# Kernel tuning notes

Measured on AMD Instinct MI355X. Metric: run time of the kernel, lower is better.

Reference implementation:

```python
import jax, jax.numpy as jnp
import numpy as np

N = 50000      # nodes
E = 800000     # edges
NFEAT = 128
NHID = 128
EPS = 1e-5     # BatchNorm eps


def setup_inputs() -> dict:
    key = jax.random.key(0)
    ks = jax.random.split(key, 16)
    def lin(k, fan_in, shape):
        return jax.random.uniform(k, shape, jnp.float32, -1.0, 1.0) / np.sqrt(fan_in)
    return {
        "x": jax.random.normal(ks[0], (N, NFEAT), jnp.float32),
        "edge_index": jax.random.randint(ks[1], (2, E), 0, N, jnp.int32),
        "edge_weight": jax.random.uniform(ks[2], (E,), jnp.float32),
        # GCNConv 1 (nfeat -> nhid)
        "W1": lin(ks[3], NFEAT, (NFEAT, NHID)), "b1": jnp.zeros((NHID,), jnp.float32),
        # GCNConv 2 (nhid -> nhid)
        "W2": lin(ks[4], NHID, (NHID, NHID)), "b2": jnp.zeros((NHID,), jnp.float32),
        # BatchNorm affine params
        "g1": jnp.ones((NHID,), jnp.float32), "be1": jnp.zeros((NHID,), jnp.float32),
        "g2": jnp.ones((NHID,), jnp.float32), "be2": jnp.zeros((NHID,), jnp.float32),
        # MLP head: fc1 (nfeat + 2*nhid -> nhid), fc2 (nhid -> 1)
        "Wf1": lin(ks[5], NFEAT + 2 * NHID, (NFEAT + 2 * NHID, NHID)),
        "bf1": lin(ks[6], NFEAT + 2 * NHID, (NHID,)),
        "Wf2": lin(ks[7], NHID, (NHID, 1)),
        "bf2": lin(ks[8], NHID, (1,)),
    }


def _gcn_conv(x, src, dst, w, W, b):
    """PyG GCNConv with add_self_loops=True and symmetric gcn_norm."""
    h = x @ W                                   # [N, out] linear first
    deg = jnp.zeros((N,), h.dtype).at[dst].add(w) + 1.0  # +1 self-loop weight
    dinv = jax.lax.rsqrt(deg)                   # deg^{-1/2}
    norm = dinv[src] * w * dinv[dst]            # [E]
    out = jnp.zeros_like(h).at[dst].add(h[src] * norm[:, None])  # scatter-add
    out = out + h * (dinv * dinv)[:, None]      # self-loop term dinv_i^2 * h_i
    return out + b


def _bn(x, g, b):  # training-mode BatchNorm1d over node dim (biased var)
    m = x.mean(axis=0)
    v = x.var(axis=0)
    return g * (x - m) * jax.lax.rsqrt(v + EPS) + b


def reference(x, edge_index, edge_weight, W1, b1, W2, b2, g1, be1, g2, be2,
              Wf1, bf1, Wf2, bf2):
    src, dst = edge_index[0], edge_index[1]
    h1 = _bn(jax.nn.relu(_gcn_conv(x, src, dst, edge_weight, W1, b1)), g1, be1)
    h2 = _bn(jax.nn.relu(_gcn_conv(h1, src, dst, edge_weight, W2, b2)), g2, be2)
    cat = jnp.concatenate([x, h1, h2], axis=1)          # [N, nfeat+2*nhid]
    out = jax.nn.relu(cat @ Wf1 + bf1)
    out = jax.nn.relu(out @ Wf2 + bf2)
    return out.reshape(-1)                              # [N]
```

## Files before the change

### kernel.cpp

```cpp
#include <hip/hip_runtime.h>
#include <hip/hip_bf16.h>
#include <hip/hip_fp16.h>

#define NN 50000
#define EE 800000
constexpr float BN_EPS = 1e-5f;

typedef float  f32x4  __attribute__((ext_vector_type(4)));
typedef short  s16x8  __attribute__((ext_vector_type(8)));
typedef __bf16 bf16x8 __attribute__((ext_vector_type(8)));

struct __align__(8) Edge { int s; float w; };

__device__ inline void split2(float f, short& h, short& l) {
    unsigned u  = __builtin_bit_cast(unsigned, f);
    unsigned hr = (u + 0x7fffu + ((u >> 16) & 1u)) >> 16;
    h = (short)hr;
    float hf = __builtin_bit_cast(float, hr << 16);
    float r  = f - hf;
    unsigned u2 = __builtin_bit_cast(unsigned, r);
    unsigned lr = (u2 + 0x7fffu + ((u2 >> 16) & 1u)) >> 16;
    l = (short)lr;
}
__device__ inline f32x4 mfma_bf16(s16x8 a, s16x8 b, f32x4 c) {
    return __builtin_amdgcn_mfma_f32_16x16x32_bf16(
        __builtin_bit_cast(bf16x8, a), __builtin_bit_cast(bf16x8, b), c, 0, 0, 0);
}

__global__ __launch_bounds__(256) void k_zero_int(int* p, int n) {
    int i = blockIdx.x * 256 + threadIdx.x;
    if (i < n) p[i] = 0;
}

__global__ __launch_bounds__(256) void k_hist_rank(const int* __restrict__ dst,
                                                   int* __restrict__ cnt,
                                                   int* __restrict__ rank) {
    int e = blockIdx.x * 256 + threadIdx.x;
    if (e < EE) rank[e] = atomicAdd(&cnt[dst[e]], 1);
}
__global__ __launch_bounds__(256) void k_scan1(const int* __restrict__ cnt,
                                               int* __restrict__ excl,
                                               int* __restrict__ blksum) {
    __shared__ int sh[256];
    int tid = threadIdx.x;
    int i = blockIdx.x * 256 + tid;
    int v = (i < NN) ? cnt[i] : 0;
    sh[tid] = v;
    __syncthreads();
    #pragma unroll
    for (int off = 1; off < 256; off <<= 1) {
        int x = (tid >= off) ? sh[tid - off] : 0;
        __syncthreads();
        sh[tid] += x;
        __syncthreads();
    }
    if (i < NN) excl[i] = sh[tid] - v;
    if (tid == 255) blksum[blockIdx.x] = sh[255];
}
__global__ __launch_bounds__(256) void k_scan2(int* blksum, int nblk) {
    __shared__ int sh[256];
    int tid = threadIdx.x;
    sh[tid] = (tid < nblk) ? blksum[tid] : 0;
    __syncthreads();
    #pragma unroll
    for (int off = 1; off < 256; off <<= 1) {
        int x = (tid >= off) ? sh[tid - off] : 0;
        __syncthreads();
        sh[tid] += x;
        __syncthreads();
    }
    if (tid < nblk) blksum[tid] = sh[tid];
}
__global__ __launch_bounds__(256) void k_scan3(const int* __restrict__ excl,
                                               const int* __restrict__ blksum,
                                               int* __restrict__ rowptr) {
    int i = blockIdx.x * 256 + threadIdx.x;
    if (i < NN)
        rowptr[i] = excl[i] + (blockIdx.x > 0 ? blksum[blockIdx.x - 1] : 0);
    if (i == 0) rowptr[NN] = EE;
}
__global__ __launch_bounds__(256) void k_place2(const int* __restrict__ src,
                                                const int* __restrict__ dst,
                                                const float* __restrict__ w,
                                                const int* __restrict__ rowptr,
                                                const int* __restrict__ rank,
                                                Edge* __restrict__ csr_e) {
    int e = blockIdx.x * 256 + threadIdx.x;
    if (e >= EE) return;
    int slot = rowptr[dst[e]] + rank[e];
    Edge ed; ed.s = src[e]; ed.w = w[e];
    csr_e[slot] = ed;
}
__global__ __launch_bounds__(256) void k_deg_dinv(const int* __restrict__ rowptr,
                                                  const Edge* __restrict__ csr_e,
                                                  float* __restrict__ dinv) {
    int i = blockIdx.x * 256 + threadIdx.x;
    if (i >= NN) return;
    int e0 = rowptr[i], e1 = rowptr[i + 1];
    float s = 1.0f;
    for (int e = e0; e < e1; e++) s += csr_e[e].w;
    dinv[i] = rsqrtf(s);
}
__global__ __launch_bounds__(256) void k_edge_coef(Edge* __restrict__ csr_e,
                                                   const float* __restrict__ dinv) {
    int e = blockIdx.x * 256 + threadIdx.x;
    if (e < EE) {
        Edge ed = csr_e[e];
        ed.w *= dinv[ed.s];
        csr_e[e] = ed;
    }
}

__global__ __launch_bounds__(256) void k_cvt_wT(const float* __restrict__ W,
                                                short* __restrict__ Th,
                                                short* __restrict__ Tl, int K) {
    int idx = blockIdx.x * 256 + threadIdx.x;
    if (idx >= K * 128) return;
    int k = idx >> 7, c = idx & 127;
    short h, l;
    split2(W[idx], h, l);
    Th[c * K + k] = h;
    Tl[c * K + k] = l;
}

__global__ __launch_bounds__(256) void gemm_mfma(const float* __restrict__ X,
                                                 const float* __restrict__ sc,
                                                 const float* __restrict__ sh,
                                                 const short* __restrict__ WTh,
                                                 const short* __restrict__ WTl,
                                                 __half* __restrict__ Y, int n) {
    __shared__ __align__(16) short As[2][64][40];
    __shared__ __align__(16) short Bs[2][128][40];
    int tid  = threadIdx.x;
    int row0 = blockIdx.x * 64;
    int w = tid >> 6, lane = tid & 63;
    int wr = w >> 1, wc = w & 1;
    int fr = lane & 15, fq = lane >> 4;
    f32x4 acc[2][4] = {};
    for (int k0 = 0; k0 < 128; k0 += 32) {
        {
            int r = tid >> 2, seg = tid & 3;
            int gr = row0 + r;
            float f[8];
            if (gr < n) {
                float4 v0 = *(const float4*)&X[(size_t)gr * 128 + k0 + seg * 8];
                float4 v1 = *(const float4*)&X[(size_t)gr * 128 + k0 + seg * 8 + 4];
                f[0]=v0.x; f[1]=v0.y; f[2]=v0.z; f[3]=v0.w;
                f[4]=v1.x; f[5]=v1.y; f[6]=v1.z; f[7]=v1.w;
            } else {
                #pragma unroll
                for (int i = 0; i < 8; i++) f[i] = 0.f;
            }
            if (sc) {
                float scv[8], shv[8];
                *(float4*)&scv[0] = *(const float4*)&sc[k0 + seg * 8];
                *(float4*)&scv[4] = *(const float4*)&sc[k0 + seg * 8 + 4];
                *(float4*)&shv[0] = *(const float4*)&sh[k0 + seg * 8];
                *(float4*)&shv[4] = *(const float4*)&sh[k0 + seg * 8 + 4];
                #pragma unroll
                for (int i = 0; i < 8; i++) f[i] = fmaf(f[i], scv[i], shv[i]);
            }
            short h[8], l[8];
            #pragma unroll
            for (int i = 0; i < 8; i++) split2(f[i], h[i], l[i]);
            *(s16x8*)&As[0][r][seg * 8] = *(s16x8*)h;
            *(s16x8*)&As[1][r][seg * 8] = *(s16x8*)l;
        }
        #pragma unroll
        for (int rd = 0; rd < 2; rd++) {
            int idx = rd * 256 + tid;
            int c = idx >> 2, seg = idx & 3;
            *(s16x8*)&Bs[0][c][seg * 8] = *(const s16x8*)&WTh[c * 128 + k0 + seg * 8];
            *(s16x8*)&Bs[1][c][seg * 8] = *(const s16x8*)&WTl[c * 128 + k0 + seg * 8];
        }
        __syncthreads();
        s16x8 ah[2], al[2], bh[4], bl[4];
        #pragma unroll
        for (int m = 0; m < 2; m++) {
            int r = wr * 32 + m * 16 + fr;
            ah[m] = *(s16x8*)&As[0][r][fq * 8];
            al[m] = *(s16x8*)&As[1][r][fq * 8];
        }
        #pragma unroll
        for (int nf = 0; nf < 4; nf++) {
            int c = wc * 64 + nf * 16 + fr;
            bh[nf] = *(s16x8*)&Bs[0][c][fq * 8];
            bl[nf] = *(s16x8*)&Bs[1][c][fq * 8];
        }
        #pragma unroll
        for (int m = 0; m < 2; m++)
            #pragma unroll
            for (int nf = 0; nf < 4; nf++) {
                acc[m][nf] = mfma_bf16(ah[m], bh[nf], acc[m][nf]);
                acc[m][nf] = mfma_bf16(ah[m], bl[nf], acc[m][nf]);
                acc[m][nf] = mfma_bf16(al[m], bh[nf], acc[m][nf]);
            }
        __syncthreads();
    }
    #pragma unroll
    for (int m = 0; m < 2; m++)
        #pragma unroll
        for (int nf = 0; nf < 4; nf++)
            #pragma unroll
            for (int j = 0; j < 4; j++) {
                int gr = row0 + wr * 32 + m * 16 + fq * 4 + j;
                int gc = wc * 64 + nf * 16 + fr;
                if (gr < n) Y[(size_t)gr * 128 + gc] = __float2half(acc[m][nf][j]);
            }
}

__global__ __launch_bounds__(256) void gemm_head_mfma(const float* __restrict__ X0,
                                                      const float* __restrict__ X1,
                                                      const float* __restrict__ X2,
                                                      const float* __restrict__ sc1,
                                                      const float* __restrict__ sh1,
                                                      const float* __restrict__ sc2,
                                                      const float* __restrict__ sh2,
                                                      const short* __restrict__ WTh,
                                                      const short* __restrict__ WTl,
                                                      const float* __restrict__ bf1,
                                                      const float* __restrict__ Wf2,
                                                      const float* __restrict__ bf2,
                                                      float* __restrict__ out) {
    __shared__ __align__(16) short As[2][64][40];
    __shared__ __align__(16) short Bs[2][128][40];
    __shared__ float red[64];
    int tid  = threadIdx.x;
    int row0 = blockIdx.x * 64;
    int w = tid >> 6, lane = tid & 63;
    int wr = w >> 1, wc = w & 1;
    int fr = lane & 15, fq = lane >> 4;
    f32x4 acc[2][4] = {};
    for (int k0 = 0; k0 < 384; k0 += 32) {
        const float* S   = (k0 < 128) ? X0 : (k0 < 256) ? X1 : X2;
        const float* scp = (k0 < 128) ? nullptr : (k0 < 256) ? sc1 : sc2;
        const float* shp = (k0 < 128) ? nullptr : (k0 < 256) ? sh1 : sh2;
        int kb = k0 & 127;
        {
            int r = tid >> 2, seg = tid & 3;
            int gr = row0 + r;
            float f[8];
            if (gr < NN) {
                float4 v0 = *(const float4*)&S[(size_t)gr * 128 + kb + seg * 8];
                float4 v1 = *(const float4*)&S[(size_t)gr * 128 + kb + seg * 8 + 4];
                f[0]=v0.x; f[1]=v0.y; f[2]=v0.z; f[3]=v0.w;
                f[4]=v1.x; f[5]=v1.y; f[6]=v1.z; f[7]=v1.w;
            } else {
                #pragma unroll
                for (int i = 0; i < 8; i++) f[i] = 0.f;
            }
            if (scp) {
                float scv[8], shv[8];
                *(float4*)&scv[0] = *(const float4*)&scp[kb + seg * 8];
                *(float4*)&scv[4] = *(const float4*)&scp[kb + seg * 8 + 4];
                *(float4*)&shv[0] = *(const float4*)&shp[kb + seg * 8];
                *(float4*)&shv[4] = *(const float4*)&shp[kb + seg * 8 + 4];
                #pragma unroll
                for (int i = 0; i < 8; i++) f[i] = fmaf(f[i], scv[i], shv[i]);
            }
            short h[8], l[8];
            #pragma unroll
            for (int i = 0; i < 8; i++) split2(f[i], h[i], l[i]);
            *(s16x8*)&As[0][r][seg * 8] = *(s16x8*)h;
            *(s16x8*)&As[1][r][seg * 8] = *(s16x8*)l;
        }
        #pragma unroll
        for (int rd = 0; rd < 2; rd++) {
            int idx = rd * 256 + tid;
            int c = idx >> 2, seg = idx & 3;
            *(s16x8*)&Bs[0][c][seg * 8] = *(const s16x8*)&WTh[c * 384 + k0 + seg * 8];
            *(s16x8*)&Bs[1][c][seg * 8] = *(const s16x8*)&WTl[c * 384 + k0 + seg * 8];
        }
        __syncthreads();
        s16x8 ah[2], al[2], bh[4], bl[4];
        #pragma unroll
        for (int m = 0; m < 2; m++) {
            int r = wr * 32 + m * 16 + fr;
            ah[m] = *(s16x8*)&As[0][r][fq * 8];
            al[m] = *(s16x8*)&As[1][r][fq * 8];
        }
        #pragma unroll
        for (int nf = 0; nf < 4; nf++) {
            int c = wc * 64 + nf * 16 + fr;
            bh[nf] = *(s16x8*)&Bs[0][c][fq * 8];
            bl[nf] = *(s16x8*)&Bs[1][c][fq * 8];
        }
        #pragma unroll
        for (int m = 0; m < 2; m++)
            #pragma unroll
            for (int nf = 0; nf < 4; nf++) {
                acc[m][nf] = mfma_bf16(ah[m], bh[nf], acc[m][nf]);
                acc[m][nf] = mfma_bf16(ah[m], bl[nf], acc[m][nf]);
                acc[m][nf] = mfma_bf16(al[m], bh[nf], acc[m][nf]);
            }
        __syncthreads();
    }
    if (tid < 64) red[tid] = 0.f;
    __syncthreads();
    float ps[2][4] = {};
    #pragma unroll
    for (int m = 0; m < 2; m++)
        #pragma unroll
        for (int nf = 0; nf < 4; nf++) {
            int gc = wc * 64 + nf * 16 + fr;
            float b1v = bf1[gc];
            float w2v = Wf2[gc];
            #pragma unroll
            for (int j = 0; j < 4; j++) {
                float u = fmaxf(acc[m][nf][j] + b1v, 0.f);
                ps[m][j] = fmaf(u, w2v, ps[m][j]);
            }
        }
    #pragma unroll
    for (int off = 1; off <= 8; off <<= 1)
        #pragma unroll
        for (int m = 0; m < 2; m++)
            #pragma unroll
            for (int j = 0; j < 4; j++)
                ps[m][j] += __shfl_xor(ps[m][j], off, 64);
    if (fr == 0) {
        #pragma unroll
        for (int m = 0; m < 2; m++)
            #pragma unroll
            for (int j = 0; j < 4; j++)
                atomicAdd(&red[wr * 32 + m * 16 + fq * 4 + j], ps[m][j]);
    }
    __syncthreads();
    if (tid < 64 && row0 + tid < NN)
        out[row0 + tid] = fmaxf(red[tid] + bf2[0], 0.f);
}

__global__ __launch_bounds__(256) void k_agg_stats(const __half* __restrict__ t,
                                                   const float* __restrict__ dinv,
                                                   const float* __restrict__ b,
                                                   const int* __restrict__ rowptr,
                                                   const Edge* __restrict__ csr_e,
                                                   float* __restrict__ h,
                                                   float* __restrict__ partS,
                                                   float* __restrict__ partSS) {
    int wv   = threadIdx.x >> 6;
    int lane = threadIdx.x & 63;
    int sub  = lane >> 4;
    int sl   = lane & 15;
    float bb[8];
    *(float4*)&bb[0] = *(const float4*)&b[sl * 8];
    *(float4*)&bb[4] = *(const float4*)&b[sl * 8 + 4];
    float sS[8] = {}, sSS[8] = {};
    #pragma unroll 1
    for (int ni = 0; ni < 8; ni++) {
        int wid = blockIdx.x * 32 + wv * 8 + ni;
        if (wid >= NN) break;
        float di = dinv[wid];
        float acc[8];
        if (sub == 0) {
            s16x8 raw = *(const s16x8*)&t[(size_t)wid * 128 + sl * 8];
            union { s16x8 r; __half2 h2[4]; } u; u.r = raw;
            #pragma unroll
            for (int i = 0; i < 4; i++) {
                float2 f = __half22float2(u.h2[i]);
                acc[2 * i]     = f.x * di;
                acc[2 * i + 1] = f.y * di;
            }
        } else {
            #pragma unroll
            for (int i = 0; i < 8; i++) acc[i] = 0.f;
        }
        int e0 = rowptr[wid], e1 = rowptr[wid + 1];
        #pragma unroll 2
        for (int e = e0; e < e1; e += 4) {
            int ee   = e + sub;
            bool v   = ee < e1;
            int idx  = v ? ee : e0;
            Edge ed  = csr_e[idx];
            float cw = v ? ed.w : 0.f;
            s16x8 raw = *(const s16x8*)&t[(size_t)ed.s * 128 + sl * 8];
            union { s16x8 r; __half2 h2[4]; } u; u.r = raw;
            #pragma unroll
            for (int i = 0; i < 4; i++) {
                float2 f = __half22float2(u.h2[i]);
                acc[2 * i]     = fmaf(f.x, cw, acc[2 * i]);
                acc[2 * i + 1] = fmaf(f.y, cw, acc[2 * i + 1]);
            }
        }
        #pragma unroll
        for (int i = 0; i < 8; i++) {
            acc[i] += __shfl_xor(acc[i], 16, 64);
            acc[i] += __shfl_xor(acc[i], 32, 64);
        }
        if (sub == 0) {
            float hv[8];
            #pragma unroll
            for (int i = 0; i < 8; i++) {
                hv[i] = fmaxf(fmaf(acc[i], di, bb[i]), 0.f);
                sS[i]  += hv[i];
                sSS[i] += hv[i] * hv[i];
            }
            *(float4*)&h[(size_t)wid * 128 + sl * 8]     = *(float4*)&hv[0];
            *(float4*)&h[(size_t)wid * 128 + sl * 8 + 4] = *(float4*)&hv[4];
        }
    }
    __shared__ float s_s[4][128], s_ss[4][128];
    if (sub == 0) {
        #pragma unroll
        for (int i = 0; i < 8; i++) {
            s_s [wv][sl * 8 + i] = sS[i];
            s_ss[wv][sl * 8 + i] = sSS[i];
        }
    }
    __syncthreads();
    if (threadIdx.x < 128) {
        int c = threadIdx.x;
        float S  = s_s [0][c] + s_s [1][c] + s_s [2][c] + s_s [3][c];
        float SS = s_ss[0][c] + s_ss[1][c] + s_ss[2][c] + s_ss[3][c];
        partS [blockIdx.x * 128 + c] = S;
        partSS[blockIdx.x * 128 + c] = SS;
    }
}

__global__ __launch_bounds__(256) void k_stats(const float* __restrict__ partS,
                                               const float* __restrict__ partSS,
                                               int nblk,
                                               const float* __restrict__ g,
                                               const float* __restrict__ be,
                                               float* __restrict__ scale,
                                               float* __restrict__ shift) {
    int c   = blockIdx.x;
    int tid = threadIdx.x;
    float s = 0.f, ss = 0.f;
    for (int b = tid; b < nblk; b += 256) {
        s  += partS [b * 128 + c];
        ss += partSS[b * 128 + c];
    }
    #pragma unroll
    for (int off = 32; off > 0; off >>= 1) {
        s  += __shfl_down(s,  off, 64);
        ss += __shfl_down(ss, off, 64);
    }
    __shared__ float sh_s[4], sh_ss[4];
    int wv = tid >> 6, lane = tid & 63;
    if (lane == 0) { sh_s[wv] = s; sh_ss[wv] = ss; }
    __syncthreads();
    if (tid == 0) {
        float S  = sh_s[0]  + sh_s[1]  + sh_s[2]  + sh_s[3];
        float SS = sh_ss[0] + sh_ss[1] + sh_ss[2] + sh_ss[3];
        float mean = S / (float)NN;
        float var  = SS / (float)NN - mean * mean;
        float sc   = g[c] * rsqrtf(var + BN_EPS);
        scale[c] = sc;
        shift[c] = be[c] - mean * sc;
    }
}

extern "C" void kernel_launch(void* const* d_in, const int* in_sizes, int n_in,
                              void* d_out, int out_size, void* d_ws, size_t ws_size,
                              hipStream_t stream) {
    const float* x   = (const float*)d_in[0];
    const int*   ei  = (const int*)d_in[1];
    const float* ew  = (const float*)d_in[2];
    const float* W1  = (const float*)d_in[3];
    const float* b1  = (const float*)d_in[4];
    const float* W2  = (const float*)d_in[5];
    const float* b2  = (const float*)d_in[6];
    const float* g1  = (const float*)d_in[7];
    const float* be1 = (const float*)d_in[8];
    const float* g2  = (const float*)d_in[9];
    const float* be2 = (const float*)d_in[10];
    const float* Wf1 = (const float*)d_in[11];
    const float* bf1 = (const float*)d_in[12];
    const float* Wf2 = (const float*)d_in[13];
    const float* bf2 = (const float*)d_in[14];
    float* out = (float*)d_out;

    const int* src = ei;
    const int* dst = ei + EE;

    const int NAGG = (NN + 31) / 32;

    float* w = (float*)d_ws;
    __half* t      = (__half*)w;  w += (size_t)NN * 64;
    float* h1      = w;  w += (size_t)NN * 128;
    float* h2      = w;  w += (size_t)NN * 128;
    float* dinv    = w;  w += 50048;
    float* partS   = w;  w += (size_t)NAGG * 128;
    float* partSS  = w;  w += (size_t)NAGG * 128;
    float* scale1  = w;  w += 128;
    float* shift1  = w;  w += 128;
    float* scale2  = w;  w += 128;
    float* shift2  = w;  w += 128;
    Edge* csr_e    = (Edge*)w;  w += 2 * (size_t)EE;
    int* iw        = (int*)w;
    int* rowptr    = iw; iw += 50056;
    int* cnt       = iw; iw += 50048;
    int* excl      = iw; iw += 50048;
    int* blksum    = iw; iw += 256;
    short* sw      = (short*)iw;
    short* W1th = sw; sw += 128 * 128;
    short* W1tl = sw; sw += 128 * 128;
    short* W2th = sw; sw += 128 * 128;
    short* W2tl = sw; sw += 128 * 128;
    short* Wfth = sw; sw += 128 * 384;
    short* Wftl = sw; sw += 128 * 384;
    int* rank = (int*)t;

    const int GN = (NN + 255) / 256;
    const int GE = (EE + 255) / 256;
    const int NBLK = (NN + 63) / 64;

    k_cvt_wT<<<(128 * 128 + 255) / 256, 256, 0, stream>>>(W1, W1th, W1tl, 128);
    k_cvt_wT<<<(128 * 128 + 255) / 256, 256, 0, stream>>>(W2, W2th, W2tl, 128);
    k_cvt_wT<<<(384 * 128 + 255) / 256, 256, 0, stream>>>(Wf1, Wfth, Wftl, 384);

    k_zero_int<<<GN, 256, 0, stream>>>(cnt, 50048);
    k_hist_rank<<<GE, 256, 0, stream>>>(dst, cnt, rank);
    k_scan1<<<GN, 256, 0, stream>>>(cnt, excl, blksum);
    k_scan2<<<1, 256, 0, stream>>>(blksum, GN);
    k_scan3<<<GN, 256, 0, stream>>>(excl, blksum, rowptr);
    k_place2<<<GE, 256, 0, stream>>>(src, dst, ew, rowptr, rank, csr_e);
    k_deg_dinv<<<GN, 256, 0, stream>>>(rowptr, csr_e, dinv);
    k_edge_coef<<<GE, 256, 0, stream>>>(csr_e, dinv);

    gemm_mfma<<<NBLK, 256, 0, stream>>>(x, nullptr, nullptr, W1th, W1tl, t, NN);
    k_agg_stats<<<NAGG, 256, 0, stream>>>(t, dinv, b1, rowptr, csr_e,
                                          h1, partS, partSS);
    k_stats<<<128, 256, 0, stream>>>(partS, partSS, NAGG, g1, be1, scale1, shift1);

    gemm_mfma<<<NBLK, 256, 0, stream>>>(h1, scale1, shift1, W2th, W2tl, t, NN);
    k_agg_stats<<<NAGG, 256, 0, stream>>>(t, dinv, b2, rowptr, csr_e,
                                          h2, partS, partSS);
    k_stats<<<128, 256, 0, stream>>>(partS, partSS, NAGG, g2, be2, scale2, shift2);

    gemm_head_mfma<<<NBLK, 256, 0, stream>>>(x, h1, h2, scale1, shift1, scale2, shift2,
                                             Wfth, Wftl, bf1, Wf2, bf2, out);
}
```

Before: 227.9 us.

## Store h1/h2 as fp16, merge weight conversions, widen aggregation blocks

Intermediate activations h1 and h2 are now written in fp16 instead of fp32, which halves their write traffic in aggregation and their read traffic in the second GEMM and the head GEMM. The three weight-conversion launches are merged into one kernel. The aggregation kernel now runs 512 threads per block with 8 waves doing 4 nodes each, and its edge loop is unrolled by 4 instead of 2. Rounding the pre-BatchNorm activations to fp16 adds quantization error to the outputs.

```diff
diff --git a/kernel.cpp b/kernel.cpp
--- a/kernel.cpp
+++ b/kernel.cpp
@@ -111,19 +111,63 @@
     }
 }
 
-__global__ __launch_bounds__(256) void k_cvt_wT(const float* __restrict__ W,
-                                                short* __restrict__ Th,
-                                                short* __restrict__ Tl, int K) {
-    int idx = blockIdx.x * 256 + threadIdx.x;
-    if (idx >= K * 128) return;
+__device__ inline void cvt_one(const float* W, short* Th, short* Tl, int idx, int K) {
     int k = idx >> 7, c = idx & 127;
     short h, l;
     split2(W[idx], h, l);
     Th[c * K + k] = h;
     Tl[c * K + k] = l;
 }
-
-__global__ __launch_bounds__(256) void gemm_mfma(const float* __restrict__ X,
+__global__ __launch_bounds__(256) void k_cvt_all(const float* __restrict__ W1,
+                                                 const float* __restrict__ W2,
+                                                 const float* __restrict__ Wf1,
+                                                 short* W1th, short* W1tl,
+                                                 short* W2th, short* W2tl,
+                                                 short* Wfth, short* Wftl) {
+    int idx = blockIdx.x * 256 + threadIdx.x;
+    if (idx < 16384)       cvt_one(W1,  W1th, W1tl, idx, 128);
+    else if (idx < 32768)  cvt_one(W2,  W2th, W2tl, idx - 16384, 128);
+    else if (idx < 81920)  cvt_one(Wf1, Wfth, Wftl, idx - 32768, 384);
+}
+
+__device__ inline void stage_a(const void* X, bool xfp16, const float* sc, const float* sh,
+                               int gr, int n, int kbase, int seg, short* h, short* l) {
+    float f[8];
+    if (gr < n) {
+        if (xfp16) {
+            const __half* Xh = (const __half*)X;
+            s16x8 raw = *(const s16x8*)&Xh[(size_t)gr * 128 + kbase + seg * 8];
+            union { s16x8 r; __half2 h2[4]; } u; u.r = raw;
+            #pragma unroll
+            for (int i = 0; i < 4; i++) {
+                float2 f2 = __half22float2(u.h2[i]);
+                f[2 * i] = f2.x; f[2 * i + 1] = f2.y;
+            }
+        } else {
+            const float* Xf = (const float*)X;
+            float4 v0 = *(const float4*)&Xf[(size_t)gr * 128 + kbase + seg * 8];
+            float4 v1 = *(const float4*)&Xf[(size_t)gr * 128 + kbase + seg * 8 + 4];
+            f[0]=v0.x; f[1]=v0.y; f[2]=v0.z; f[3]=v0.w;
+            f[4]=v1.x; f[5]=v1.y; f[6]=v1.z; f[7]=v1.w;
+        }
+    } else {
+        #pragma unroll
+        for (int i = 0; i < 8; i++) f[i] = 0.f;
+    }
+    if (sc) {
+        float scv[8], shv[8];
+        *(float4*)&scv[0] = *(const float4*)&sc[kbase + seg * 8];
+        *(float4*)&scv[4] = *(const float4*)&sc[kbase + seg * 8 + 4];
+        *(float4*)&shv[0] = *(const float4*)&sh[kbase + seg * 8];
+        *(float4*)&shv[4] = *(const float4*)&sh[kbase + seg * 8 + 4];
+        #pragma unroll
+        for (int i = 0; i < 8; i++) f[i] = fmaf(f[i], scv[i], shv[i]);
+    }
+    #pragma unroll
+    for (int i = 0; i < 8; i++) split2(f[i], h[i], l[i]);
+}
+
+__global__ __launch_bounds__(256) void gemm_mfma(const void* __restrict__ X, int xfp16,
                                                  const float* __restrict__ sc,
                                                  const float* __restrict__ sh,
                                                  const short* __restrict__ WTh,
@@ -140,29 +184,8 @@
     for (int k0 = 0; k0 < 128; k0 += 32) {
         {
             int r = tid >> 2, seg = tid & 3;
-            int gr = row0 + r;
-            float f[8];
-            if (gr < n) {
-                float4 v0 = *(const float4*)&X[(size_t)gr * 128 + k0 + seg * 8];
-                float4 v1 = *(const float4*)&X[(size_t)gr * 128 + k0 + seg * 8 + 4];
-                f[0]=v0.x; f[1]=v0.y; f[2]=v0.z; f[3]=v0.w;
-                f[4]=v1.x; f[5]=v1.y; f[6]=v1.z; f[7]=v1.w;
-            } else {
-                #pragma unroll
-                for (int i = 0; i < 8; i++) f[i] = 0.f;
-            }
-            if (sc) {
-                float scv[8], shv[8];
-                *(float4*)&scv[0] = *(const float4*)&sc[k0 + seg * 8];
-                *(float4*)&scv[4] = *(const float4*)&sc[k0 + seg * 8 + 4];
-                *(float4*)&shv[0] = *(const float4*)&sh[k0 + seg * 8];
-                *(float4*)&shv[4] = *(const float4*)&sh[k0 + seg * 8 + 4];
-                #pragma unroll
-                for (int i = 0; i < 8; i++) f[i] = fmaf(f[i], scv[i], shv[i]);
-            }
             short h[8], l[8];
-            #pragma unroll
-            for (int i = 0; i < 8; i++) split2(f[i], h[i], l[i]);
+            stage_a(X, xfp16 != 0, sc, sh, row0 + r, n, k0, seg, h, l);
             *(s16x8*)&As[0][r][seg * 8] = *(s16x8*)h;
             *(s16x8*)&As[1][r][seg * 8] = *(s16x8*)l;
         }
@@ -210,8 +233,8 @@
 }
 
 __global__ __launch_bounds__(256) void gemm_head_mfma(const float* __restrict__ X0,
-                                                      const float* __restrict__ X1,
-                                                      const float* __restrict__ X2,
+                                                      const __half* __restrict__ X1,
+                                                      const __half* __restrict__ X2,
                                                       const float* __restrict__ sc1,
                                                       const float* __restrict__ sh1,
                                                       const float* __restrict__ sc2,
@@ -232,35 +255,15 @@
     int fr = lane & 15, fq = lane >> 4;
     f32x4 acc[2][4] = {};
     for (int k0 = 0; k0 < 384; k0 += 32) {
-        const float* S   = (k0 < 128) ? X0 : (k0 < 256) ? X1 : X2;
-        const float* scp = (k0 < 128) ? nullptr : (k0 < 256) ? sc1 : sc2;
-        const float* shp = (k0 < 128) ? nullptr : (k0 < 256) ? sh1 : sh2;
+        const void*  S     = (k0 < 128) ? (const void*)X0 : (k0 < 256) ? (const void*)X1 : (const void*)X2;
+        bool         sfp16 = (k0 >= 128);
+        const float* scp   = (k0 < 128) ? nullptr : (k0 < 256) ? sc1 : sc2;
+        const float* shp   = (k0 < 128) ? nullptr : (k0 < 256) ? sh1 : sh2;
         int kb = k0 & 127;
         {
             int r = tid >> 2, seg = tid & 3;
-            int gr = row0 + r;
-            float f[8];
-            if (gr < NN) {
-                float4 v0 = *(const float4*)&S[(size_t)gr * 128 + kb + seg * 8];
-                float4 v1 = *(const float4*)&S[(size_t)gr * 128 + kb + seg * 8 + 4];
-                f[0]=v0.x; f[1]=v0.y; f[2]=v0.z; f[3]=v0.w;
-                f[4]=v1.x; f[5]=v1.y; f[6]=v1.z; f[7]=v1.w;
-            } else {
-                #pragma unroll
-                for (int i = 0; i < 8; i++) f[i] = 0.f;
-            }
-            if (scp) {
-                float scv[8], shv[8];
-                *(float4*)&scv[0] = *(const float4*)&scp[kb + seg * 8];
-                *(float4*)&scv[4] = *(const float4*)&scp[kb + seg * 8 + 4];
-                *(float4*)&shv[0] = *(const float4*)&shp[kb + seg * 8];
-                *(float4*)&shv[4] = *(const float4*)&shp[kb + seg * 8 + 4];
-                #pragma unroll
-                for (int i = 0; i < 8; i++) f[i] = fmaf(f[i], scv[i], shv[i]);
-            }
             short h[8], l[8];
-            #pragma unroll
-            for (int i = 0; i < 8; i++) split2(f[i], h[i], l[i]);
+            stage_a(S, sfp16, scp, shp, row0 + r, NN, kb, seg, h, l);
             *(s16x8*)&As[0][r][seg * 8] = *(s16x8*)h;
             *(s16x8*)&As[1][r][seg * 8] = *(s16x8*)l;
         }
@@ -330,12 +333,12 @@
         out[row0 + tid] = fmaxf(red[tid] + bf2[0], 0.f);
 }
 
-__global__ __launch_bounds__(256) void k_agg_stats(const __half* __restrict__ t,
+__global__ __launch_bounds__(512) void k_agg_stats(const __half* __restrict__ t,
                                                    const float* __restrict__ dinv,
                                                    const float* __restrict__ b,
                                                    const int* __restrict__ rowptr,
                                                    const Edge* __restrict__ csr_e,
-                                                   float* __restrict__ h,
+                                                   __half* __restrict__ h,
                                                    float* __restrict__ partS,
                                                    float* __restrict__ partSS) {
     int wv   = threadIdx.x >> 6;
@@ -347,8 +350,8 @@
     *(float4*)&bb[4] = *(const float4*)&b[sl * 8 + 4];
     float sS[8] = {}, sSS[8] = {};
     #pragma unroll 1
-    for (int ni = 0; ni < 8; ni++) {
-        int wid = blockIdx.x * 32 + wv * 8 + ni;
+    for (int ni = 0; ni < 4; ni++) {
+        int wid = blockIdx.x * 32 + wv * 4 + ni;
         if (wid >= NN) break;
         float di = dinv[wid];
         float acc[8];
@@ -366,12 +369,11 @@
             for (int i = 0; i < 8; i++) acc[i] = 0.f;
         }
         int e0 = rowptr[wid], e1 = rowptr[wid + 1];
-        #pragma unroll 2
+        #pragma unroll 4
         for (int e = e0; e < e1; e += 4) {
             int ee   = e + sub;
             bool v   = ee < e1;
-            int idx  = v ? ee : e0;
-            Edge ed  = csr_e[idx];
+            Edge ed  = csr_e[v ? ee : e0];
             float cw = v ? ed.w : 0.f;
             s16x8 raw = *(const s16x8*)&t[(size_t)ed.s * 128 + sl * 8];
             union { s16x8 r; __half2 h2[4]; } u; u.r = raw;
@@ -389,17 +391,20 @@
         }
         if (sub == 0) {
             float hv[8];
+            union { s16x8 r; __half2 h2[4]; } o;
             #pragma unroll
             for (int i = 0; i < 8; i++) {
                 hv[i] = fmaxf(fmaf(acc[i], di, bb[i]), 0.f);
                 sS[i]  += hv[i];
                 sSS[i] += hv[i] * hv[i];
             }
-            *(float4*)&h[(size_t)wid * 128 + sl * 8]     = *(float4*)&hv[0];
-            *(float4*)&h[(size_t)wid * 128 + sl * 8 + 4] = *(float4*)&hv[4];
-        }
-    }
-    __shared__ float s_s[4][128], s_ss[4][128];
+            #pragma unroll
+            for (int i = 0; i < 4; i++)
+                o.h2[i] = __floats2half2_rn(hv[2 * i], hv[2 * i + 1]);
+            *(s16x8*)&h[(size_t)wid * 128 + sl * 8] = o.r;
+        }
+    }
+    __shared__ float s_s[8][128], s_ss[8][128];
     if (sub == 0) {
         #pragma unroll
         for (int i = 0; i < 8; i++) {
@@ -410,8 +415,9 @@
     __syncthreads();
     if (threadIdx.x < 128) {
         int c = threadIdx.x;
-        float S  = s_s [0][c] + s_s [1][c] + s_s [2][c] + s_s [3][c];
-        float SS = s_ss[0][c] + s_ss[1][c] + s_ss[2][c] + s_ss[3][c];
+        float S = 0.f, SS = 0.f;
+        #pragma unroll
+        for (int k = 0; k < 8; k++) { S += s_s[k][c]; SS += s_ss[k][c]; }
         partS [blockIdx.x * 128 + c] = S;
         partSS[blockIdx.x * 128 + c] = SS;
     }
@@ -478,8 +484,8 @@
 
     float* w = (float*)d_ws;
     __half* t      = (__half*)w;  w += (size_t)NN * 64;
-    float* h1      = w;  w += (size_t)NN * 128;
-    float* h2      = w;  w += (size_t)NN * 128;
+    __half* h1     = (__half*)w;  w += (size_t)NN * 64;
+    __half* h2     = (__half*)w;  w += (size_t)NN * 64;
     float* dinv    = w;  w += 50048;
     float* partS   = w;  w += (size_t)NAGG * 128;
     float* partSS  = w;  w += (size_t)NAGG * 128;
@@ -506,10 +512,8 @@
     const int GE = (EE + 255) / 256;
     const int NBLK = (NN + 63) / 64;
 
-    k_cvt_wT<<<(128 * 128 + 255) / 256, 256, 0, stream>>>(W1, W1th, W1tl, 128);
-    k_cvt_wT<<<(128 * 128 + 255) / 256, 256, 0, stream>>>(W2, W2th, W2tl, 128);
-    k_cvt_wT<<<(384 * 128 + 255) / 256, 256, 0, stream>>>(Wf1, Wfth, Wftl, 384);
-
+    k_cvt_all<<<(81920 + 255) / 256, 256, 0, stream>>>(W1, W2, Wf1, W1th, W1tl,
+                                                       W2th, W2tl, Wfth, Wftl);
     k_zero_int<<<GN, 256, 0, stream>>>(cnt, 50048);
     k_hist_rank<<<GE, 256, 0, stream>>>(dst, cnt, rank);
     k_scan1<<<GN, 256, 0, stream>>>(cnt, excl, blksum);
@@ -519,14 +523,12 @@
     k_deg_dinv<<<GN, 256, 0, stream>>>(rowptr, csr_e, dinv);
     k_edge_coef<<<GE, 256, 0, stream>>>(csr_e, dinv);
 
-    gemm_mfma<<<NBLK, 256, 0, stream>>>(x, nullptr, nullptr, W1th, W1tl, t, NN);
-    k_agg_stats<<<NAGG, 256, 0, stream>>>(t, dinv, b1, rowptr, csr_e,
-                                          h1, partS, partSS);
+    gemm_mfma<<<NBLK, 256, 0, stream>>>(x, 0, nullptr, nullptr, W1th, W1tl, t, NN);
+    k_agg_stats<<<NAGG, 512, 0, stream>>>(t, dinv, b1, rowptr, csr_e, h1, partS, partSS);
     k_stats<<<128, 256, 0, stream>>>(partS, partSS, NAGG, g1, be1, scale1, shift1);
 
-    gemm_mfma<<<NBLK, 256, 0, stream>>>(h1, scale1, shift1, W2th, W2tl, t, NN);
-    k_agg_stats<<<NAGG, 256, 0, stream>>>(t, dinv, b2, rowptr, csr_e,
-                                          h2, partS, partSS);
+    gemm_mfma<<<NBLK, 256, 0, stream>>>(h1, 1, scale1, shift1, W2th, W2tl, t, NN);
+    k_agg_stats<<<NAGG, 512, 0, stream>>>(t, dinv, b2, rowptr, csr_e, h2, partS, partSS);
     k_stats<<<128, 256, 0, stream>>>(partS, partSS, NAGG, g2, be2, scale2, shift2);
 
     gemm_head_mfma<<<NBLK, 256, 0, stream>>>(x, h1, h2, scale1, shift1, scale2, shift2,
```

Result: slower. 249.2 us (+9.3%).
